# Optimization experiments

Measured on AMD Instinct MI355X. Metric: run time of the kernel, lower is better.

Reference implementation:

```python
import jax, jax.numpy as jnp
import numpy as np

N_STATE = 1024
N_HEAD = 16
HEAD_DIM = N_STATE // N_HEAD


def setup_inputs() -> dict:
    key = jax.random.key(0)
    ks = jax.random.split(key, 8)
    B, S = 8, 1500
    x = jax.random.normal(ks[0], (B, S, N_STATE), dtype=jnp.float32)
    # additive causal mask (0 on/below diagonal, -inf above), broadcast over B,H
    neg = jnp.float32(-1e9)
    mask = jnp.where(jnp.tril(jnp.ones((S, S), dtype=bool)), 0.0, neg).astype(jnp.float32)
    s = 0.02
    Wq = jax.random.normal(ks[1], (N_STATE, N_STATE), dtype=jnp.float32) * s
    bq = jnp.zeros((N_STATE,), dtype=jnp.float32)
    Wk = jax.random.normal(ks[2], (N_STATE, N_STATE), dtype=jnp.float32) * s
    Wv = jax.random.normal(ks[3], (N_STATE, N_STATE), dtype=jnp.float32) * s
    bv = jnp.zeros((N_STATE,), dtype=jnp.float32)
    Wo = jax.random.normal(ks[4], (N_STATE, N_STATE), dtype=jnp.float32) * s
    bo = jnp.zeros((N_STATE,), dtype=jnp.float32)
    return {"x": x, "mask": mask, "Wq": Wq, "bq": bq, "Wk": Wk, "Wv": Wv, "bv": bv, "Wo": Wo, "bo": bo}


def reference(x, mask, Wq, bq, Wk, Wv, bv, Wo, bo):
    B, S, _ = x.shape
    # linear projections (torch Linear: x @ W^T + b); W stored as [out, in]
    q = x @ Wq.T + bq
    k = x @ Wk.T
    v = x @ Wv.T + bv
    # [B, H, S, D]
    q = q.reshape(B, S, N_HEAD, HEAD_DIM).transpose(0, 2, 1, 3)
    k = k.reshape(B, S, N_HEAD, HEAD_DIM).transpose(0, 2, 1, 3)
    v = v.reshape(B, S, N_HEAD, HEAD_DIM).transpose(0, 2, 1, 3)
    scale = 1.0 / np.sqrt(HEAD_DIM).astype(np.float32)
    scores = jnp.einsum('bhqd,bhkd->bhqk', q, k) * scale + mask
    attn = jax.nn.softmax(scores, axis=-1)
    out = jnp.einsum('bhqk,bhkd->bhqd', attn, v)
    out = out.transpose(0, 2, 1, 3).reshape(B, S, N_STATE)
    return out @ Wo.T + bo
```

## Files before the change

### kernel.cpp

```cpp
#include <hip/hip_runtime.h>
#include <hip/hip_bf16.h>

#define N_STATE 1024
#define N_HEAD  16
#define D_HEAD  64
#define BATCH   8
#define SEQ     1500
#define ROWS    (BATCH*SEQ)
#define SVP     1536
#define MTILES  94

#define BM 128
#define BN 128
#define BK 32
#define BK2 64

typedef __bf16 bf16x8 __attribute__((ext_vector_type(8)));
typedef __bf16 bf16x4 __attribute__((ext_vector_type(4)));
typedef float  f32x4  __attribute__((ext_vector_type(4)));

__device__ __forceinline__ f32x4 mfma16(bf16x8 a, bf16x8 b, f32x4 c) {
  return __builtin_amdgcn_mfma_f32_16x16x32_bf16(a, b, c, 0, 0, 0);
}

__device__ __forceinline__ void gl_lds16(const void* g, void* l) {
  __builtin_amdgcn_global_load_lds(
      (const __attribute__((address_space(1))) unsigned int*)g,
      (__attribute__((address_space(3))) unsigned int*)l, 16, 0, 0);
}

__device__ __forceinline__ void bar() {
  __builtin_amdgcn_sched_barrier(0);
  __builtin_amdgcn_s_barrier();
  __builtin_amdgcn_sched_barrier(0);
  asm volatile("" ::: "memory");
}

__global__ __launch_bounds__(256)
void cvt_all(const float* __restrict__ x,  const float* __restrict__ wq,
             const float* __restrict__ wk, const float* __restrict__ wv,
             const float* __restrict__ wo,
             __bf16* __restrict__ xb, __bf16* __restrict__ wb)
{
  const int which = blockIdx.y;
  const float* src;
  __bf16* dst;
  size_t n;
  if (which == 0) { src = x; dst = xb; n = (size_t)ROWS * N_STATE; }
  else {
    src = (which == 1) ? wq : (which == 2) ? wk : (which == 3) ? wv : wo;
    dst = wb + (size_t)(which - 1) * N_STATE * N_STATE;
    n = (size_t)N_STATE * N_STATE;
  }
  const size_t stride = (size_t)gridDim.x * 256 * 4;
  for (size_t i = ((size_t)blockIdx.x * 256 + threadIdx.x) * 4; i < n; i += stride) {
    const f32x4 v = *(const f32x4*)(src + i);
    bf16x4 c; c[0]=(__bf16)v[0]; c[1]=(__bf16)v[1]; c[2]=(__bf16)v[2]; c[3]=(__bf16)v[3];
    *(bf16x4*)(dst + i) = c;
  }
}

__global__ __launch_bounds__(512, 4)
void qkv_db(const __bf16* __restrict__ xb, const __bf16* __restrict__ wb,
            const float* __restrict__ bq, const float* __restrict__ bv,
            __bf16* __restrict__ q_ws, __bf16* __restrict__ k_ws,
            __bf16* __restrict__ vt_ws)
{
  const int xcd = blockIdx.x & 7;
  const int jj  = blockIdx.x >> 3;
  const int nt  = jj & 7;
  const int mt  = (jj >> 3) * 8 + xcd;
  if (mt >= MTILES) return;

  __shared__ __bf16 lA[2][BM * BK2];
  __shared__ __bf16 lB[2][BN * BK2];
  const int which = blockIdx.z;
  const __bf16* W = wb + (size_t)which * N_STATE * N_STATE;

  const int tid = threadIdx.x;
  const int lane = tid & 63, wave = tid >> 6;
  const int l15 = lane & 15, quad = lane >> 4;
  const int wr = wave & 1, wc = wave >> 1;

  f32x4 acc[4][2] = {};

  auto stage = [&](int kt) {
    const int k0 = kt * BK2;
    __bf16* dA = (__bf16*)lA[kt & 1];
    __bf16* dB = (__bf16*)lB[kt & 1];
#pragma unroll
    for (int t = 0; t < 2; ++t) {
      const int c = wave * 2 + t;
      const int s = c * 64 + lane;
      const int row = s >> 3;
      const int sw  = (lane & 7) ^ (row & 7);
      const int ga = min(mt * BM + row, ROWS - 1);
      gl_lds16(xb + (size_t)ga * N_STATE + k0 + sw * 8, dA + c * 512);
      const int gb = nt * BN + row;
      gl_lds16(W + (size_t)gb * N_STATE + k0 + sw * 8, dB + c * 512);
    }
  };

  stage(0);
  for (int kt = 0; kt < N_STATE / BK2; ++kt) {
    if (kt < N_STATE / BK2 - 1) {
      stage(kt + 1);
      asm volatile("s_waitcnt vmcnt(4)" ::: "memory");
    } else {
      asm volatile("s_waitcnt vmcnt(0)" ::: "memory");
    }
    bar();
    const __bf16* cA = lA[kt & 1];
    const __bf16* cB = lB[kt & 1];
#pragma unroll
    for (int h = 0; h < 2; ++h) {
      bf16x8 af[4], bfr[2];
#pragma unroll
      for (int i = 0; i < 4; ++i) {
        const int ra = wr * 64 + i * 16 + l15;
        af[i] = *(const bf16x8*)&cA[ra * BK2 + (((h * 4 + quad) ^ (ra & 7)) * 8)];
      }
#pragma unroll
      for (int j = 0; j < 2; ++j) {
        const int rb = wc * 32 + j * 16 + l15;
        bfr[j] = *(const bf16x8*)&cB[rb * BK2 + (((h * 4 + quad) ^ (rb & 7)) * 8)];
      }
      if (which != 2) {
#pragma unroll
        for (int i = 0; i < 4; ++i)
#pragma unroll
          for (int j = 0; j < 2; ++j)
            acc[i][j] = mfma16(af[i], bfr[j], acc[i][j]);
      } else {
#pragma unroll
        for (int i = 0; i < 4; ++i)
#pragma unroll
          for (int j = 0; j < 2; ++j)
            acc[i][j] = mfma16(bfr[j], af[i], acc[i][j]);
      }
    }
    bar();
  }

  if (which != 2) {
#pragma unroll
    for (int i = 0; i < 4; ++i) {
      const int mrow = mt * BM + wr * 64 + i * 16 + quad * 4;
#pragma unroll
      for (int j = 0; j < 2; ++j) {
        const int col = nt * BN + wc * 32 + j * 16 + l15;
        const int h = col >> 6, d = col & 63;
        const float badd = (which == 0) ? bq[col] : 0.0f;
        __bf16* dst = (which == 0) ? q_ws : k_ws;
#pragma unroll
        for (int r = 0; r < 4; ++r) {
          const int row = mrow + r;
          if (row < ROWS) {
            const int b = row / SEQ, s = row % SEQ;
            dst[(((size_t)(b * N_HEAD + h)) * SEQ + s) * D_HEAD + d] =
                (__bf16)(acc[i][j][r] + badd);
          }
        }
      }
    }
  } else {
#pragma unroll
    for (int i = 0; i < 4; ++i) {
      const int sg = mt * BM + wr * 64 + i * 16 + l15;
      const bool valid = sg < ROWS;
      const int b = sg / SEQ, srow = sg % SEQ;
#pragma unroll
      for (int j = 0; j < 2; ++j) {
        const int dbase = nt * BN + wc * 32 + j * 16 + quad * 4;
#pragma unroll
        for (int r = 0; r < 4; ++r) {
          const int d = dbase + r;
          const int h = d >> 6, dd = d & 63;
          if (valid)
            vt_ws[(((size_t)(b * N_HEAD + h)) * D_HEAD + dd) * SVP + srow] =
                (__bf16)(acc[i][j][r] + bv[d]);
        }
      }
    }
  }
}

__global__ __launch_bounds__(512, 4)
void out_db(const __bf16* __restrict__ a_in, const __bf16* __restrict__ wob,
            const float* __restrict__ bo, float* __restrict__ out)
{
  const int xcd = blockIdx.x & 7;
  const int jj  = blockIdx.x >> 3;
  const int nt  = jj & 7;
  const int mt  = (jj >> 3) * 8 + xcd;
  if (mt >= MTILES) return;

  __shared__ __bf16 lA[2][BM * BK2];
  __shared__ __bf16 lB[2][BN * BK2];
  const int tid = threadIdx.x;
  const int lane = tid & 63, wave = tid >> 6;
  const int l15 = lane & 15, quad = lane >> 4;
  const int wr = wave & 1, wc = wave >> 1;

  f32x4 acc[4][2] = {};

  auto stage = [&](int kt) {
    const int k0 = kt * BK2;
    __bf16* dA = (__bf16*)lA[kt & 1];
    __bf16* dB = (__bf16*)lB[kt & 1];
#pragma unroll
    for (int t = 0; t < 2; ++t) {
      const int c = wave * 2 + t;
      const int s = c * 64 + lane;
      const int row = s >> 3;
      const int sw  = (lane & 7) ^ (row & 7);
      const int ga = min(mt * BM + row, ROWS - 1);
      gl_lds16(a_in + (size_t)ga * N_STATE + k0 + sw * 8, dA + c * 512);
      const int gb = nt * BN + row;
      gl_lds16(wob + (size_t)gb * N_STATE + k0 + sw * 8, dB + c * 512);
    }
  };

  stage(0);
  for (int kt = 0; kt < N_STATE / BK2; ++kt) {
    if (kt < N_STATE / BK2 - 1) {
      stage(kt + 1);
      asm volatile("s_waitcnt vmcnt(4)" ::: "memory");
    } else {
      asm volatile("s_waitcnt vmcnt(0)" ::: "memory");
    }
    bar();
    const __bf16* cA = lA[kt & 1];
    const __bf16* cB = lB[kt & 1];
#pragma unroll
    for (int h = 0; h < 2; ++h) {
      bf16x8 af[4], bfr[2];
#pragma unroll
      for (int i = 0; i < 4; ++i) {
        const int ra = wr * 64 + i * 16 + l15;
        af[i] = *(const bf16x8*)&cA[ra * BK2 + (((h * 4 + quad) ^ (ra & 7)) * 8)];
      }
#pragma unroll
      for (int j = 0; j < 2; ++j) {
        const int rb = wc * 32 + j * 16 + l15;
        bfr[j] = *(const bf16x8*)&cB[rb * BK2 + (((h * 4 + quad) ^ (rb & 7)) * 8)];
      }
#pragma unroll
      for (int i = 0; i < 4; ++i)
#pragma unroll
        for (int j = 0; j < 2; ++j)
          acc[i][j] = mfma16(af[i], bfr[j], acc[i][j]);
    }
    bar();
  }

#pragma unroll
  for (int i = 0; i < 4; ++i) {
    const int mrow = mt * BM + wr * 64 + i * 16 + quad * 4;
#pragma unroll
    for (int j = 0; j < 2; ++j) {
      const int col = nt * BN + wc * 32 + j * 16 + l15;
      const float badd = bo[col];
#pragma unroll
      for (int r = 0; r < 4; ++r) {
        const int row = mrow + r;
        if (row < ROWS)
          out[(size_t)row * N_STATE + col] = acc[i][j][r] + badd;
      }
    }
  }
}

__global__ __launch_bounds__(256)
void qkv_gemm(const float* __restrict__ x,
              const float* __restrict__ Wq, const float* __restrict__ bq,
              const float* __restrict__ Wk,
              const float* __restrict__ Wv, const float* __restrict__ bv,
              __bf16* __restrict__ q_ws, __bf16* __restrict__ k_ws,
              __bf16* __restrict__ vt_ws)
{
  __shared__ __bf16 lA[BM * BK];
  __shared__ __bf16 lB[BN * BK];
  const int which = blockIdx.z;
  const float* W    = (which == 0) ? Wq : (which == 1) ? Wk : Wv;
  const float* bias = (which == 0) ? bq : (which == 2) ? bv : nullptr;

  const int mt = blockIdx.x, nt = blockIdx.y;
  const int tid = threadIdx.x;
  const int lane = tid & 63, wave = tid >> 6;
  const int l15 = lane & 15, quad = lane >> 4;
  const int wr = wave >> 1, wc = wave & 1;

  f32x4 acc[4][4] = {};

  for (int k0 = 0; k0 < N_STATE; k0 += BK) {
#pragma unroll
    for (int it = 0; it < 4; ++it) {
      const int s = tid + it * 256;
      const int row = s >> 3, seg = s & 7;
      const int ga = min(mt * BM + row, ROWS - 1);
      const f32x4 va = *(const f32x4*)(x + (size_t)ga * N_STATE + k0 + seg * 4);
      bf16x4 ca; ca[0]=(__bf16)va[0]; ca[1]=(__bf16)va[1];
                 ca[2]=(__bf16)va[2]; ca[3]=(__bf16)va[3];
      *(bf16x4*)&lA[row * BK + seg * 4] = ca;
      const int gb = nt * BM + row;
      const f32x4 vb = *(const f32x4*)(W + (size_t)gb * N_STATE + k0 + seg * 4);
      bf16x4 cb; cb[0]=(__bf16)vb[0]; cb[1]=(__bf16)vb[1];
                 cb[2]=(__bf16)vb[2]; cb[3]=(__bf16)vb[3];
      *(bf16x4*)&lB[row * BK + seg * 4] = cb;
    }
    __syncthreads();
    bf16x8 af[4], bfr[4];
#pragma unroll
    for (int i = 0; i < 4; ++i) {
      af[i]  = *(const bf16x8*)&lA[(wr * 64 + i * 16 + l15) * BK + quad * 8];
      bfr[i] = *(const bf16x8*)&lB[(wc * 64 + i * 16 + l15) * BK + quad * 8];
    }
    if (which != 2) {
#pragma unroll
      for (int i = 0; i < 4; ++i)
#pragma unroll
        for (int j = 0; j < 4; ++j)
          acc[i][j] = mfma16(af[i], bfr[j], acc[i][j]);
    } else {
#pragma unroll
      for (int i = 0; i < 4; ++i)
#pragma unroll
        for (int j = 0; j < 4; ++j)
          acc[i][j] = mfma16(bfr[j], af[i], acc[i][j]);
    }
    __syncthreads();
  }

  if (which != 2) {
#pragma unroll
    for (int i = 0; i < 4; ++i) {
      const int mrow = mt * BM + wr * 64 + i * 16 + quad * 4;
#pragma unroll
      for (int j = 0; j < 4; ++j) {
        const int col = nt * BN + wc * 64 + j * 16 + l15;
        const int h = col >> 6, d = col & 63;
        const float badd = bias ? bias[col] : 0.0f;
        __bf16* dst = (which == 0) ? q_ws : k_ws;
#pragma unroll
        for (int r = 0; r < 4; ++r) {
          const int row = mrow + r;
          if (row < ROWS) {
            const int b = row / SEQ, s = row % SEQ;
            dst[(((size_t)(b * N_HEAD + h)) * SEQ + s) * D_HEAD + d] =
                (__bf16)(acc[i][j][r] + badd);
          }
        }
      }
    }
  } else {
#pragma unroll
    for (int i = 0; i < 4; ++i) {
      const int sg = mt * BM + wr * 64 + i * 16 + l15;
      const bool valid = sg < ROWS;
      const int b = sg / SEQ, srow = sg % SEQ;
#pragma unroll
      for (int j = 0; j < 4; ++j) {
        const int dbase = nt * BN + wc * 64 + j * 16 + quad * 4;
#pragma unroll
        for (int r = 0; r < 4; ++r) {
          const int d = dbase + r;
          const int h = d >> 6, dd = d & 63;
          if (valid)
            vt_ws[(((size_t)(b * N_HEAD + h)) * D_HEAD + dd) * SVP + srow] =
                (__bf16)(acc[i][j][r] + bias[d]);
        }
      }
    }
  }
}

__global__ __launch_bounds__(256)
void flash_attn(const __bf16* __restrict__ q_ws, const __bf16* __restrict__ k_ws,
                const __bf16* __restrict__ vt_ws, __bf16* __restrict__ attn)
{
  __shared__ __align__(16) __bf16 lK[8 * 512];
  __shared__ __align__(16) __bf16 lV[8 * 512];
  __shared__ __align__(16) __bf16 lP[4 * 16 * 72];
  const int bh = blockIdx.x;
  const int qt = gridDim.y - 1 - blockIdx.y;
  const int tid = threadIdx.x, lane = tid & 63, wave = tid >> 6;
  const int l15 = lane & 15, quad = lane >> 4;
  const __bf16* Q  = q_ws  + (size_t)bh * SEQ * D_HEAD;
  const __bf16* K  = k_ws  + (size_t)bh * SEQ * D_HEAD;
  const __bf16* Vt = vt_ws + (size_t)bh * D_HEAD * SVP;
  __bf16* lPw = lP + wave * 16 * 72;

  const int q0 = qt * 64, wq0 = q0 + wave * 16;
  const int qload = min(wq0 + l15, SEQ - 1);
  const bf16x8 qa0 = *(const bf16x8*)(Q + (size_t)qload * D_HEAD + quad * 8);
  const bf16x8 qa1 = *(const bf16x8*)(Q + (size_t)qload * D_HEAD + 32 + quad * 8);

  const float NEG = -1.0e30f;
  const float scale = 0.125f;
  const int query = wq0 + l15;
  f32x4 o[4] = {};
  float m_i = NEG, l_i = 0.0f;

  const int kmax = min(q0 + 63, SEQ - 1);
  const int wqmax = wq0 + 15;

  for (int kt = 0; kt <= kmax; kt += 64) {
#pragma unroll
    for (int t = 0; t < 2; ++t) {
      const int c = wave * 2 + t;
      const int gk = min(kt + lane, SEQ - 1);
      gl_lds16(K + (size_t)gk * D_HEAD + c * 8, (__bf16*)lK + c * 512);
      gl_lds16(Vt + (size_t)lane * SVP + kt + c * 8, (__bf16*)lV + c * 512);
    }
    __syncthreads();

    if (kt <= wqmax) {
      f32x4 sg[4] = {};
      __builtin_amdgcn_s_setprio(1);
#pragma unroll
      for (int g = 0; g < 4; ++g) {
        const bf16x8 k0 = *(const bf16x8*)&lK[quad * 512 + (g * 16 + l15) * 8];
        const bf16x8 k1 = *(const bf16x8*)&lK[(4 + quad) * 512 + (g * 16 + l15) * 8];
        sg[g] = mfma16(k0, qa0, sg[g]);
        sg[g] = mfma16(k1, qa1, sg[g]);
      }
      __builtin_amdgcn_s_setprio(0);
      const bool fullvis = (kt + 63 <= wq0) && (kt + 63 < SEQ);
      float tmax = NEG;
#pragma unroll
      for (int g = 0; g < 4; ++g)
#pragma unroll
        for (int r = 0; r < 4; ++r) {
          float v = sg[g][r] * scale;
          if (!fullvis) {
            const int key = kt + g * 16 + quad * 4 + r;
            v = (key <= query && key < SEQ) ? v : NEG;
          }
          sg[g][r] = v;
          tmax = fmaxf(tmax, v);
        }
      tmax = fmaxf(tmax, __shfl_xor(tmax, 16));
      tmax = fmaxf(tmax, __shfl_xor(tmax, 32));
      if (!__all(tmax <= m_i + 8.0f)) {
        const float mnew = fmaxf(m_i, tmax);
        const float alpha = __expf(m_i - mnew);
        l_i *= alpha;
#pragma unroll
        for (int nn = 0; nn < 4; ++nn)
#pragma unroll
          for (int r = 0; r < 4; ++r) o[nn][r] *= alpha;
        m_i = mnew;
      }
      float rsum = 0.0f;
#pragma unroll
      for (int g = 0; g < 4; ++g) {
        bf16x4 pk;
#pragma unroll
        for (int r = 0; r < 4; ++r) {
          const float e = __expf(sg[g][r] - m_i);
          rsum += e;
          pk[r] = (__bf16)e;
        }
        *(bf16x4*)&lPw[l15 * 72 + g * 16 + quad * 4] = pk;
      }
      rsum += __shfl_xor(rsum, 16);
      rsum += __shfl_xor(rsum, 32);
      l_i += rsum;

      __builtin_amdgcn_s_setprio(1);
#pragma unroll
      for (int h = 0; h < 2; ++h) {
        const bf16x8 pb = *(const bf16x8*)&lPw[l15 * 72 + h * 32 + quad * 8];
#pragma unroll
        for (int nn = 0; nn < 4; ++nn) {
          const bf16x8 va =
              *(const bf16x8*)&lV[(h * 4 + quad) * 512 + (nn * 16 + l15) * 8];
          o[nn] = mfma16(va, pb, o[nn]);
        }
      }
      __builtin_amdgcn_s_setprio(0);
    }
    __syncthreads();
  }

  const int b = bh >> 4, hh = bh & 15;
  if (query < SEQ) {
    const float inv = 1.0f / l_i;
#pragma unroll
    for (int nn = 0; nn < 4; ++nn) {
      bf16x4 ov;
#pragma unroll
      for (int r = 0; r < 4; ++r) ov[r] = (__bf16)(o[nn][r] * inv);
      *(bf16x4*)&attn[(((size_t)(b * SEQ + query)) * N_HEAD + hh) * D_HEAD +
                      nn * 16 + quad * 4] = ov;
    }
  }
}

__global__ __launch_bounds__(256)
void out_gemm(const __bf16* __restrict__ a_in, const float* __restrict__ Wo,
              const float* __restrict__ bo, float* __restrict__ out)
{
  __shared__ __bf16 lA[BM * BK];
  __shared__ __bf16 lB[BN * BK];
  const int mt = blockIdx.x, nt = blockIdx.y;
  const int tid = threadIdx.x;
  const int lane = tid & 63, wave = tid >> 6;
  const int l15 = lane & 15, quad = lane >> 4;
  const int wr = wave >> 1, wc = wave & 1;

  f32x4 acc[4][4] = {};

  for (int k0 = 0; k0 < N_STATE; k0 += BK) {
#pragma unroll
    for (int it = 0; it < 2; ++it) {
      const int s = tid + it * 256;
      const int row = s >> 2, seg = s & 3;
      const int ga = min(mt * BM + row, ROWS - 1);
      *(bf16x8*)&lA[row * BK + seg * 8] =
          *(const bf16x8*)(a_in + (size_t)ga * N_STATE + k0 + seg * 8);
    }
#pragma unroll
    for (int it = 0; it < 4; ++it) {
      const int s = tid + it * 256;
      const int row = s >> 3, seg = s & 7;
      const int gb = nt * BM + row;
      const f32x4 vb = *(const f32x4*)(Wo + (size_t)gb * N_STATE + k0 + seg * 4);
      bf16x4 cb; cb[0]=(__bf16)vb[0]; cb[1]=(__bf16)vb[1];
                 cb[2]=(__bf16)vb[2]; cb[3]=(__bf16)vb[3];
      *(bf16x4*)&lB[row * BK + seg * 4] = cb;
    }
    __syncthreads();
    bf16x8 af[4], bfr[4];
#pragma unroll
    for (int i = 0; i < 4; ++i) {
      af[i]  = *(const bf16x8*)&lA[(wr * 64 + i * 16 + l15) * BK + quad * 8];
      bfr[i] = *(const bf16x8*)&lB[(wc * 64 + i * 16 + l15) * BK + quad * 8];
    }
#pragma unroll
    for (int i = 0; i < 4; ++i)
#pragma unroll
      for (int j = 0; j < 4; ++j)
        acc[i][j] = mfma16(af[i], bfr[j], acc[i][j]);
    __syncthreads();
  }

#pragma unroll
  for (int i = 0; i < 4; ++i) {
    const int mrow = mt * BM + wr * 64 + i * 16 + quad * 4;
#pragma unroll
    for (int j = 0; j < 4; ++j) {
      const int col = nt * BN + wc * 64 + j * 16 + l15;
      const float badd = bo[col];
#pragma unroll
      for (int r = 0; r < 4; ++r) {
        const int row = mrow + r;
        if (row < ROWS)
          out[(size_t)row * N_STATE + col] = acc[i][j][r] + badd;
      }
    }
  }
}

extern "C" void kernel_launch(void* const* d_in, const int* in_sizes, int n_in,
                              void* d_out, int out_size, void* d_ws, size_t ws_size,
                              hipStream_t stream) {
  const float* x  = (const float*)d_in[0];
  const float* Wq = (const float*)d_in[2];
  const float* bq = (const float*)d_in[3];
  const float* Wk = (const float*)d_in[4];
  const float* Wv = (const float*)d_in[5];
  const float* bv = (const float*)d_in[6];
  const float* Wo = (const float*)d_in[7];
  const float* bo = (const float*)d_in[8];
  float* out = (float*)d_out;

  const size_t chunk  = (size_t)ROWS * N_STATE;
  const size_t vchunk = (size_t)BATCH * N_HEAD * D_HEAD * SVP;
  const size_t wchunk = (size_t)4 * N_STATE * N_STATE;
  __bf16* q_ws  = (__bf16*)d_ws;
  __bf16* k_ws  = q_ws + chunk;
  __bf16* vt_ws = k_ws + chunk;
  __bf16* attn  = vt_ws + vchunk;
  __bf16* xb    = attn;
  __bf16* wb    = attn + chunk;
  const size_t need = (3 * chunk + vchunk + wchunk) * sizeof(__bf16);

  const int MT = (ROWS + BM - 1) / BM;
  if (ws_size >= need) {
    cvt_all<<<dim3(1024, 5), 256, 0, stream>>>(x, Wq, Wk, Wv, Wo, xb, wb);
    qkv_db<<<dim3(768, 1, 3), 512, 0, stream>>>(
        xb, wb, bq, bv, q_ws, k_ws, vt_ws);
    flash_attn<<<dim3(BATCH * N_HEAD, (SEQ + 63) / 64), 256, 0, stream>>>(
        q_ws, k_ws, vt_ws, attn);
    out_db<<<dim3(768, 1, 1), 512, 0, stream>>>(
        attn, wb + (size_t)3 * N_STATE * N_STATE, bo, out);
  } else {
    qkv_gemm<<<dim3(MT, N_STATE / BN, 3), 256, 0, stream>>>(
        x, Wq, bq, Wk, Wv, bv, q_ws, k_ws, vt_ws);
    flash_attn<<<dim3(BATCH * N_HEAD, (SEQ + 63) / 64), 256, 0, stream>>>(
        q_ws, k_ws, vt_ws, attn);
    out_gemm<<<dim3(MT, N_STATE / BN), 256, 0, stream>>>(attn, Wo, bo, out);
  }
}
```

Measured before the change: 359.8 us.

## Enlarge QKV GEMM tile to 256x256 with interleaved staged prefetch

```diff
diff --git a/kernel.cpp b/kernel.cpp
--- a/kernel.cpp
+++ b/kernel.cpp
@@ -9,6 +9,7 @@
 #define ROWS    (BATCH*SEQ)
 #define SVP     1536
 #define MTILES  94
+#define MT256   47
 
 #define BM 128
 #define BN 128
@@ -60,20 +61,20 @@
   }
 }
 
-__global__ __launch_bounds__(512, 4)
-void qkv_db(const __bf16* __restrict__ xb, const __bf16* __restrict__ wb,
-            const float* __restrict__ bq, const float* __restrict__ bv,
-            __bf16* __restrict__ q_ws, __bf16* __restrict__ k_ws,
-            __bf16* __restrict__ vt_ws)
+__global__ __launch_bounds__(512, 2)
+void qkv_big(const __bf16* __restrict__ xb, const __bf16* __restrict__ wb,
+             const float* __restrict__ bq, const float* __restrict__ bv,
+             __bf16* __restrict__ q_ws, __bf16* __restrict__ k_ws,
+             __bf16* __restrict__ vt_ws)
 {
   const int xcd = blockIdx.x & 7;
   const int jj  = blockIdx.x >> 3;
-  const int nt  = jj & 7;
-  const int mt  = (jj >> 3) * 8 + xcd;
-  if (mt >= MTILES) return;
-
-  __shared__ __bf16 lA[2][BM * BK2];
-  __shared__ __bf16 lB[2][BN * BK2];
+  const int nt  = jj & 3;
+  const int mt  = (jj >> 2) * 8 + xcd;
+  if (mt >= MT256) return;
+
+  __shared__ __bf16 lA[2][256 * 64];
+  __shared__ __bf16 lB[2][256 * 64];
   const int which = blockIdx.z;
   const __bf16* W = wb + (size_t)which * N_STATE * N_STATE;
 
@@ -82,73 +83,102 @@
   const int l15 = lane & 15, quad = lane >> 4;
   const int wr = wave & 1, wc = wave >> 1;
 
-  f32x4 acc[4][2] = {};
-
-  auto stage = [&](int kt) {
-    const int k0 = kt * BK2;
-    __bf16* dA = (__bf16*)lA[kt & 1];
-    __bf16* dB = (__bf16*)lB[kt & 1];
+  f32x4 acc[8][4] = {};
+
+  auto stage_half = [&](int kt, int st) {
+    const int k0 = kt * 64;
+    const int buf = kt & 1;
 #pragma unroll
     for (int t = 0; t < 2; ++t) {
-      const int c = wave * 2 + t;
+      const int c = (st & 1) * 16 + wave * 2 + t;
       const int s = c * 64 + lane;
       const int row = s >> 3;
       const int sw  = (lane & 7) ^ (row & 7);
-      const int ga = min(mt * BM + row, ROWS - 1);
-      gl_lds16(xb + (size_t)ga * N_STATE + k0 + sw * 8, dA + c * 512);
-      const int gb = nt * BN + row;
-      gl_lds16(W + (size_t)gb * N_STATE + k0 + sw * 8, dB + c * 512);
+      if (st < 2) {
+        const int ga = min(mt * 256 + row, ROWS - 1);
+        gl_lds16(xb + (size_t)ga * N_STATE + k0 + sw * 8,
+                 (__bf16*)lA[buf] + c * 512);
+      } else {
+        const int gb = nt * 256 + row;
+        gl_lds16(W + (size_t)gb * N_STATE + k0 + sw * 8,
+                 (__bf16*)lB[buf] + c * 512);
+      }
     }
   };
 
-  stage(0);
-  for (int kt = 0; kt < N_STATE / BK2; ++kt) {
-    if (kt < N_STATE / BK2 - 1) {
-      stage(kt + 1);
-      asm volatile("s_waitcnt vmcnt(4)" ::: "memory");
+  stage_half(0, 0); stage_half(0, 1); stage_half(0, 2); stage_half(0, 3);
+
+  for (int kt = 0; kt < N_STATE / 64; ++kt) {
+    const __bf16* cA = lA[kt & 1];
+    const __bf16* cB = lB[kt & 1];
+    const bool pf = (kt < N_STATE / 64 - 1);
+
+    bf16x8 af[4][2], b0[2][2], b1[2][2];
+
+    auto read_a = [&](bf16x8 (&a)[4][2], int qm) {
+#pragma unroll
+      for (int i = 0; i < 4; ++i) {
+        const int ra = wr * 128 + qm * 64 + i * 16 + l15;
+#pragma unroll
+        for (int kh = 0; kh < 2; ++kh)
+          a[i][kh] = *(const bf16x8*)&cA[ra * 64 + (((kh * 4 + quad) ^ (ra & 7)) * 8)];
+      }
+    };
+    auto read_b = [&](bf16x8 (&b)[2][2], int qn) {
+#pragma unroll
+      for (int j = 0; j < 2; ++j) {
+        const int rb = wc * 64 + qn * 32 + j * 16 + l15;
+#pragma unroll
+        for (int kh = 0; kh < 2; ++kh)
+          b[j][kh] = *(const bf16x8*)&cB[rb * 64 + (((kh * 4 + quad) ^ (rb & 7)) * 8)];
+      }
+    };
+    auto do_quad = [&](bf16x8 (&a)[4][2], bf16x8 (&b)[2][2], int qm, int qn) {
+      __builtin_amdgcn_s_setprio(1);
+#pragma unroll
+      for (int kh = 0; kh < 2; ++kh)
+#pragma unroll
+        for (int i = 0; i < 4; ++i)
+#pragma unroll
+          for (int j = 0; j < 2; ++j) {
+            if (which != 2)
+              acc[qm * 4 + i][qn * 2 + j] =
+                  mfma16(a[i][kh], b[j][kh], acc[qm * 4 + i][qn * 2 + j]);
+            else
+              acc[qm * 4 + i][qn * 2 + j] =
+                  mfma16(b[j][kh], a[i][kh], acc[qm * 4 + i][qn * 2 + j]);
+          }
+      __builtin_amdgcn_s_setprio(0);
+    };
+
+    if (pf) {
+      stage_half(kt + 1, 0);
+      asm volatile("s_waitcnt vmcnt(2)" ::: "memory");
     } else {
       asm volatile("s_waitcnt vmcnt(0)" ::: "memory");
     }
     bar();
-    const __bf16* cA = lA[kt & 1];
-    const __bf16* cB = lB[kt & 1];
-#pragma unroll
-    for (int h = 0; h < 2; ++h) {
-      bf16x8 af[4], bfr[2];
-#pragma unroll
-      for (int i = 0; i < 4; ++i) {
-        const int ra = wr * 64 + i * 16 + l15;
-        af[i] = *(const bf16x8*)&cA[ra * BK2 + (((h * 4 + quad) ^ (ra & 7)) * 8)];
-      }
-#pragma unroll
-      for (int j = 0; j < 2; ++j) {
-        const int rb = wc * 32 + j * 16 + l15;
-        bfr[j] = *(const bf16x8*)&cB[rb * BK2 + (((h * 4 + quad) ^ (rb & 7)) * 8)];
-      }
-      if (which != 2) {
-#pragma unroll
-        for (int i = 0; i < 4; ++i)
-#pragma unroll
-          for (int j = 0; j < 2; ++j)
-            acc[i][j] = mfma16(af[i], bfr[j], acc[i][j]);
-      } else {
-#pragma unroll
-        for (int i = 0; i < 4; ++i)
-#pragma unroll
-          for (int j = 0; j < 2; ++j)
-            acc[i][j] = mfma16(bfr[j], af[i], acc[i][j]);
-      }
-    }
+    read_a(af, 0);
+    read_b(b0, 0);
+    do_quad(af, b0, 0, 0);
+    if (pf) stage_half(kt + 1, 1);
+    read_b(b1, 1);
+    do_quad(af, b1, 0, 1);
+    if (pf) stage_half(kt + 1, 2);
+    read_a(af, 1);
+    do_quad(af, b0, 1, 0);
+    if (pf) stage_half(kt + 1, 3);
+    do_quad(af, b1, 1, 1);
     bar();
   }
 
   if (which != 2) {
 #pragma unroll
-    for (int i = 0; i < 4; ++i) {
-      const int mrow = mt * BM + wr * 64 + i * 16 + quad * 4;
-#pragma unroll
-      for (int j = 0; j < 2; ++j) {
-        const int col = nt * BN + wc * 32 + j * 16 + l15;
+    for (int I = 0; I < 8; ++I) {
+      const int mrow = mt * 256 + wr * 128 + I * 16 + quad * 4;
+#pragma unroll
+      for (int J = 0; J < 4; ++J) {
+        const int col = nt * 256 + wc * 64 + J * 16 + l15;
         const int h = col >> 6, d = col & 63;
         const float badd = (which == 0) ? bq[col] : 0.0f;
         __bf16* dst = (which == 0) ? q_ws : k_ws;
@@ -158,27 +188,27 @@
           if (row < ROWS) {
             const int b = row / SEQ, s = row % SEQ;
             dst[(((size_t)(b * N_HEAD + h)) * SEQ + s) * D_HEAD + d] =
-                (__bf16)(acc[i][j][r] + badd);
+                (__bf16)(acc[I][J][r] + badd);
           }
         }
       }
     }
   } else {
 #pragma unroll
-    for (int i = 0; i < 4; ++i) {
-      const int sg = mt * BM + wr * 64 + i * 16 + l15;
+    for (int I = 0; I < 8; ++I) {
+      const int sg = mt * 256 + wr * 128 + I * 16 + l15;
       const bool valid = sg < ROWS;
       const int b = sg / SEQ, srow = sg % SEQ;
 #pragma unroll
-      for (int j = 0; j < 2; ++j) {
-        const int dbase = nt * BN + wc * 32 + j * 16 + quad * 4;
+      for (int J = 0; J < 4; ++J) {
+        const int dbase = nt * 256 + wc * 64 + J * 16 + quad * 4;
 #pragma unroll
         for (int r = 0; r < 4; ++r) {
           const int d = dbase + r;
           const int h = d >> 6, dd = d & 63;
           if (valid)
             vt_ws[(((size_t)(b * N_HEAD + h)) * D_HEAD + dd) * SVP + srow] =
-                (__bf16)(acc[i][j][r] + bv[d]);
+                (__bf16)(acc[I][J][r] + bv[d]);
         }
       }
     }
@@ -590,7 +620,7 @@
   const int MT = (ROWS + BM - 1) / BM;
   if (ws_size >= need) {
     cvt_all<<<dim3(1024, 5), 256, 0, stream>>>(x, Wq, Wk, Wv, Wo, xb, wb);
-    qkv_db<<<dim3(768, 1, 3), 512, 0, stream>>>(
+    qkv_big<<<dim3(192, 1, 3), 512, 0, stream>>>(
         xb, wb, bq, bv, q_ws, k_ws, vt_ws);
     flash_attn<<<dim3(BATCH * N_HEAD, (SEQ + 63) / 64), 256, 0, stream>>>(
         q_ws, k_ws, vt_ws, attn);
```

Result: slower. 410.7 us (+14.2%).
